# Performance work log

Measured on AMD Instinct MI355X. Metric: run time of the kernel, lower is better.

Reference implementation:

```python
import jax, jax.numpy as jnp
import numpy as np

H = 10            # forecast_horizon
DT = H / (H - 1)  # torchdiffeq 'rk4' steps on the linspace(0, H, H) grid
HID = 64


def setup_inputs() -> dict:
    key = jax.random.key(0)
    ks = jax.random.split(key, 7)
    x = jax.random.normal(ks[0], (1, 4096, 24), dtype=jnp.float32)
    # GCNConv params: out = A_hat @ (X W) + b
    W1 = jax.random.normal(ks[1], (1, HID), dtype=jnp.float32) * 0.5
    b1 = jax.random.normal(ks[2], (HID,), dtype=jnp.float32) * 0.1
    W2 = jax.random.normal(ks[3], (HID, HID), dtype=jnp.float32) * (1.0 / np.sqrt(HID))
    b2 = jax.random.normal(ks[4], (HID,), dtype=jnp.float32) * 0.1
    W3 = jax.random.normal(ks[5], (HID, 1), dtype=jnp.float32) * (1.0 / np.sqrt(HID))
    b3 = jax.random.normal(ks[6], (1,), dtype=jnp.float32) * 0.1
    return {"x": x, "W1": W1, "b1": b1, "W2": W2, "b2": b2, "W3": W3, "b3": b3}


def reference(x, W1, b1, W2, b2, W3, b3):
    B, N, T = x.shape  # B = 1, so the B*N state rows coincide with the N graph nodes
    M = B * N
    y0 = x[:, :, -1].reshape(M, 1)  # initial ODE state (B*N, F=1)

    def f(y):
        # GCNConv on a fully-connected graph with self-loops: every degree = M,
        # so A_hat = (1/M) * ones(M, M) and A_hat @ Z is the broadcasted mean of Z.
        h = jnp.mean(y @ W1, axis=0, keepdims=True) + b1  # (1, HID)
        h = jnp.tanh(h)
        h = jnp.mean(h @ W2, axis=0, keepdims=True) + b2  # rows identical -> mean is identity
        h = jnp.tanh(h)
        h = jnp.mean(h @ W3, axis=0, keepdims=True) + b3  # (1, 1)
        return jnp.broadcast_to(h, (M, h.shape[-1]))      # (M, 1)

    def step(y, _):
        # torchdiffeq fixed-step 'rk4' = 3/8-rule RK4 (rk4_alt_step_func); f is autonomous
        k1 = f(y)
        k2 = f(y + DT * k1 / 3.0)
        k3 = f(y + DT * (k2 - k1 / 3.0))
        k4 = f(y + DT * (k1 - k2 + k3))
        y = y + DT * (k1 + 3.0 * k2 + 3.0 * k3 + k4) / 8.0
        return y, y

    _, ys = jax.lax.scan(step, y0, None, length=H - 1)
    preds = jnp.concatenate([y0[None], ys], axis=0)  # (H, M, 1)
    # view(H, B, N, F).permute(1, 3, 2, 0).squeeze(1) with F=1 -> (B, N, H)
    out = preds.reshape(H, B, N).transpose(1, 2, 0)
    return out
```

## Files before the change

### kernel.cpp

```cpp
#include <hip/hip_runtime.h>

typedef _Float16 half2_t __attribute__((ext_vector_type(2)));
typedef _Float16 half8_t __attribute__((ext_vector_type(8)));

constexpr int M_NODES = 4096;
constexpr int T_IN    = 24;
constexpr int HIDN    = 64;
constexpr int HOR     = 10;

__device__ __forceinline__ float fast_tanh(float x) {
    float e = __builtin_amdgcn_exp2f(x * 2.8853900817779268f);
    return 1.f - 2.f * __builtin_amdgcn_rcpf(e + 1.f);
}

__device__ __forceinline__ float fdot2f16(half2_t a, half2_t b, float c) {
#if __has_builtin(__builtin_amdgcn_fdot2)
    return __builtin_amdgcn_fdot2(a, b, c, false);
#else
    return fmaf((float)a[0], (float)b[0], fmaf((float)a[1], (float)b[1], c));
#endif
}

template<int CTRL, int ROW_MASK>
__device__ __forceinline__ float dpp_add(float v) {
    int t = __builtin_amdgcn_update_dpp(0, __float_as_int(v), CTRL, ROW_MASK, 0xf, true);
    return v + __int_as_float(t);
}
__device__ __forceinline__ float wave_allsum(float v) {
    v = dpp_add<0x111, 0xf>(v);
    v = dpp_add<0x112, 0xf>(v);
    v = dpp_add<0x114, 0xf>(v);
    v = dpp_add<0x118, 0xf>(v);
    v = dpp_add<0x142, 0xa>(v);
    v = dpp_add<0x143, 0xc>(v);
    return __int_as_float(__builtin_amdgcn_readlane(__float_as_int(v), 63));
}

__global__ __launch_bounds__(256, 1) void fused_gode_kernel(
    const float* __restrict__ x,
    const float* __restrict__ W1, const float* __restrict__ b1,
    const float* __restrict__ W2, const float* __restrict__ b2,
    const float* __restrict__ W3, const float* __restrict__ b3,
    float* __restrict__ out)
{
    const int tid  = threadIdx.x;
    const int lane = tid & 63;
    const int wid  = tid >> 6;

    __shared__ float y0s[M_NODES];
    __shared__ float psum[256];
    __shared__ __align__(16) _Float16 h1h[HIDN];
    __shared__ float cs[HOR];

    float w2f[HIDN];
    float w1 = 0.f, bb1 = 0.f, bb2 = 0.f, w3 = 0.f, bb3 = 0.f;
    if (wid == 0) {
        #pragma unroll
        for (int i = 0; i < HIDN; ++i) w2f[i] = W2[i * HIDN + lane];
        w1  = W1[lane];
        bb1 = b1[lane];
        bb2 = b2[lane];
        w3  = W3[lane];
        bb3 = b3[0];
    }

    float msum = 0.f;
    #pragma unroll
    for (int k = 0; k < M_NODES / 256; ++k) {
        int n = tid + 256 * k;
        float v = x[n * T_IN + (T_IN - 1)];
        y0s[n] = v;
        msum += v;
    }
    psum[tid] = msum;
    __syncthreads();

    if (wid == 0) {
        float s = psum[lane] + psum[lane + 64] + psum[lane + 128] + psum[lane + 192];
        float mu = wave_allsum(s) * (1.0f / (float)M_NODES);

        half2_t w2h[HIDN / 2];
        #pragma unroll
        for (int i = 0; i < HIDN; i += 2)
            w2h[i / 2] = half2_t{(_Float16)w2f[i], (_Float16)w2f[i + 1]};

        auto feval = [&](float arg) -> float {
            float h1 = fast_tanh(arg);
            h1h[lane] = (_Float16)h1;
            __builtin_amdgcn_wave_barrier();
            const half8_t* hv = (const half8_t*)h1h;
            float acc[8];
            #pragma unroll
            for (int r = 0; r < 8; ++r) {
                half8_t u = hv[r];
                half2_t p0{u[0], u[1]}, p1{u[2], u[3]}, p2{u[4], u[5]}, p3{u[6], u[7]};
                float a = fdot2f16(p0, w2h[4 * r + 0], 0.f);
                a = fdot2f16(p1, w2h[4 * r + 1], a);
                a = fdot2f16(p2, w2h[4 * r + 2], a);
                acc[r] = fdot2f16(p3, w2h[4 * r + 3], a);
            }
            float h2 = fast_tanh((((acc[0] + acc[1]) + (acc[2] + acc[3])) +
                                  ((acc[4] + acc[5]) + (acc[6] + acc[7]))) + bb2);
            __builtin_amdgcn_wave_barrier();
            return wave_allsum(h2 * w3) + bb3;
        };

        const float DT  = (float)HOR / (float)(HOR - 1);
        const float dw  = DT * w1;
        const float dw3 = (DT * (1.f / 3.f)) * w1;

        float c = 0.f;
        if (lane == 0) cs[0] = 0.f;
        for (int t = 1; t < HOR; ++t) {
            float base = fmaf(mu, w1, bb1);
            float k1 = feval(base);
            float k2 = feval(fmaf(k1, dw3, base));
            float k3 = feval(fmaf(k2, dw, fmaf(k1, -dw3, base)));
            float k4 = feval(fmaf(k3, dw, fmaf(k1 - k2, dw, base)));
            float d  = DT * (k1 + 3.f * k2 + 3.f * k3 + k4) * 0.125f;
            mu += d;
            c  += d;
            if (lane == 0) cs[t] = c;
        }
    }
    __syncthreads();

    float4* out4 = (float4*)out;
    constexpr int NV4 = M_NODES * HOR / 4;
    #pragma unroll
    for (int k = 0; k < NV4 / 256; ++k) {
        int idx = tid + 256 * k;
        int e = idx * 4;
        int n = e / 10;
        int h = e - n * 10;
        float4 v;
        v.x = y0s[n] + cs[h]; if (++h == 10) { h = 0; ++n; }
        v.y = y0s[n] + cs[h]; if (++h == 10) { h = 0; ++n; }
        v.z = y0s[n] + cs[h]; if (++h == 10) { h = 0; ++n; }
        v.w = y0s[n] + cs[h];
        out4[idx] = v;
    }
}

extern "C" void kernel_launch(void* const* d_in, const int* in_sizes, int n_in,
                              void* d_out, int out_size, void* d_ws, size_t ws_size,
                              hipStream_t stream) {
    const float* x  = (const float*)d_in[0];
    const float* W1 = (const float*)d_in[1];
    const float* b1 = (const float*)d_in[2];
    const float* W2 = (const float*)d_in[3];
    const float* b2 = (const float*)d_in[4];
    const float* W3 = (const float*)d_in[5];
    const float* b3 = (const float*)d_in[6];
    float* out = (float*)d_out;

    fused_gode_kernel<<<1, 256, 0, stream>>>(x, W1, b1, W2, b2, W3, b3, out);
}
```

Baseline: 19.47 us.

## Split into partial-sum kernel and multi-block ODE solve with distributed output writes

```diff
diff --git a/kernel.cpp b/kernel.cpp
--- a/kernel.cpp
+++ b/kernel.cpp
@@ -7,6 +7,8 @@
 constexpr int T_IN    = 24;
 constexpr int HIDN    = 64;
 constexpr int HOR     = 10;
+constexpr int NB1     = 16;
+constexpr int NB2     = 64;
 
 __device__ __forceinline__ float fast_tanh(float x) {
     float e = __builtin_amdgcn_exp2f(x * 2.8853900817779268f);
@@ -36,8 +38,21 @@
     return __int_as_float(__builtin_amdgcn_readlane(__float_as_int(v), 63));
 }
 
-__global__ __launch_bounds__(256, 1) void fused_gode_kernel(
-    const float* __restrict__ x,
+__global__ __launch_bounds__(256) void partial_sum_kernel(
+    const float* __restrict__ x, float* __restrict__ partials)
+{
+    const int tid = threadIdx.x;
+    const int n   = blockIdx.x * 256 + tid;
+    float v = x[n * T_IN + (T_IN - 1)];
+    float s = wave_allsum(v);
+    __shared__ float ps[4];
+    if ((tid & 63) == 0) ps[tid >> 6] = s;
+    __syncthreads();
+    if (tid == 0) partials[blockIdx.x] = (ps[0] + ps[1]) + (ps[2] + ps[3]);
+}
+
+__global__ __launch_bounds__(256, 1) void ode_write_kernel(
+    const float* __restrict__ x, const float* __restrict__ partials,
     const float* __restrict__ W1, const float* __restrict__ b1,
     const float* __restrict__ W2, const float* __restrict__ b2,
     const float* __restrict__ W3, const float* __restrict__ b3,
@@ -47,37 +62,28 @@
     const int lane = tid & 63;
     const int wid  = tid >> 6;
 
-    __shared__ float y0s[M_NODES];
-    __shared__ float psum[256];
+    __shared__ float cs[HOR];
     __shared__ __align__(16) _Float16 h1h[HIDN];
-    __shared__ float cs[HOR];
+    __shared__ float ys[64 + 1];
 
-    float w2f[HIDN];
-    float w1 = 0.f, bb1 = 0.f, bb2 = 0.f, w3 = 0.f, bb3 = 0.f;
+    const int nbase = blockIdx.x * (M_NODES / NB2);
+    if (tid < 64) ys[tid] = x[(nbase + tid) * T_IN + (T_IN - 1)];
+
     if (wid == 0) {
+        float w2f[HIDN];
         #pragma unroll
         for (int i = 0; i < HIDN; ++i) w2f[i] = W2[i * HIDN + lane];
-        w1  = W1[lane];
-        bb1 = b1[lane];
-        bb2 = b2[lane];
-        w3  = W3[lane];
-        bb3 = b3[0];
-    }
+        const float w1  = W1[lane];
+        const float bb1 = b1[lane];
+        const float bb2 = b2[lane];
+        const float w3  = W3[lane];
+        const float bb3 = b3[0];
 
-    float msum = 0.f;
-    #pragma unroll
-    for (int k = 0; k < M_NODES / 256; ++k) {
-        int n = tid + 256 * k;
-        float v = x[n * T_IN + (T_IN - 1)];
-        y0s[n] = v;
-        msum += v;
-    }
-    psum[tid] = msum;
-    __syncthreads();
-
-    if (wid == 0) {
-        float s = psum[lane] + psum[lane + 64] + psum[lane + 128] + psum[lane + 192];
-        float mu = wave_allsum(s) * (1.0f / (float)M_NODES);
+        const float4* p4 = (const float4*)partials;
+        float4 pa = p4[0], pb = p4[1], pc = p4[2], pd = p4[3];
+        float mu = (((pa.x + pa.y) + (pa.z + pa.w)) + ((pb.x + pb.y) + (pb.z + pb.w)) +
+                    ((pc.x + pc.y) + (pc.z + pc.w)) + ((pd.x + pd.y) + (pd.z + pd.w)))
+                   * (1.0f / (float)M_NODES);
 
         half2_t w2h[HIDN / 2];
         #pragma unroll
@@ -125,20 +131,17 @@
     }
     __syncthreads();
 
-    float4* out4 = (float4*)out;
-    constexpr int NV4 = M_NODES * HOR / 4;
-    #pragma unroll
-    for (int k = 0; k < NV4 / 256; ++k) {
-        int idx = tid + 256 * k;
-        int e = idx * 4;
+    constexpr int NF4 = (M_NODES / NB2) * HOR / 4;
+    if (tid < NF4) {
+        int e = tid * 4;
         int n = e / 10;
         int h = e - n * 10;
         float4 v;
-        v.x = y0s[n] + cs[h]; if (++h == 10) { h = 0; ++n; }
-        v.y = y0s[n] + cs[h]; if (++h == 10) { h = 0; ++n; }
-        v.z = y0s[n] + cs[h]; if (++h == 10) { h = 0; ++n; }
-        v.w = y0s[n] + cs[h];
-        out4[idx] = v;
+        v.x = ys[n] + cs[h]; if (++h == 10) { h = 0; ++n; }
+        v.y = ys[n] + cs[h]; if (++h == 10) { h = 0; ++n; }
+        v.z = ys[n] + cs[h]; if (++h == 10) { h = 0; ++n; }
+        v.w = ys[n] + cs[h];
+        ((float4*)(out + nbase * HOR))[tid] = v;
     }
 }
 
@@ -152,7 +155,9 @@
     const float* b2 = (const float*)d_in[4];
     const float* W3 = (const float*)d_in[5];
     const float* b3 = (const float*)d_in[6];
-    float* out = (float*)d_out;
+    float* out      = (float*)d_out;
+    float* partials = (float*)d_ws;
 
-    fused_gode_kernel<<<1, 256, 0, stream>>>(x, W1, b1, W2, b2, W3, b3, out);
+    partial_sum_kernel<<<NB1, 256, 0, stream>>>(x, partials);
+    ode_write_kernel<<<NB2, 256, 0, stream>>>(x, partials, W1, b1, W2, b2, W3, b3, out);
 }
```

New measurement: 19.88 us. +2.1%, slower.

## Replicate ODE solve across 64 blocks, each writing its own node slice

Applied to the files above, without the earlier changes.

```diff
diff --git a/kernel.cpp b/kernel.cpp
--- a/kernel.cpp
+++ b/kernel.cpp
@@ -7,6 +7,7 @@
 constexpr int T_IN    = 24;
 constexpr int HIDN    = 64;
 constexpr int HOR     = 10;
+constexpr int NB      = 64;
 
 __device__ __forceinline__ float fast_tanh(float x) {
     float e = __builtin_amdgcn_exp2f(x * 2.8853900817779268f);
@@ -47,10 +48,12 @@
     const int lane = tid & 63;
     const int wid  = tid >> 6;
 
-    __shared__ float y0s[M_NODES];
     __shared__ float psum[256];
+    __shared__ float cs[HOR];
     __shared__ __align__(16) _Float16 h1h[HIDN];
-    __shared__ float cs[HOR];
+    __shared__ float ys[64 + 1];
+
+    const int nbase = blockIdx.x * (M_NODES / NB);
 
     float w2f[HIDN];
     float w1 = 0.f, bb1 = 0.f, bb2 = 0.f, w3 = 0.f, bb3 = 0.f;
@@ -63,21 +66,18 @@
         w3  = W3[lane];
         bb3 = b3[0];
     }
+    if (wid == 1) ys[lane] = x[(nbase + lane) * T_IN + (T_IN - 1)];
 
-    float msum = 0.f;
+    float s = 0.f;
     #pragma unroll
-    for (int k = 0; k < M_NODES / 256; ++k) {
-        int n = tid + 256 * k;
-        float v = x[n * T_IN + (T_IN - 1)];
-        y0s[n] = v;
-        msum += v;
-    }
-    psum[tid] = msum;
+    for (int k = 0; k < M_NODES / 256; ++k)
+        s += x[(tid + 256 * k) * T_IN + (T_IN - 1)];
+    psum[tid] = s;
     __syncthreads();
 
     if (wid == 0) {
-        float s = psum[lane] + psum[lane + 64] + psum[lane + 128] + psum[lane + 192];
-        float mu = wave_allsum(s) * (1.0f / (float)M_NODES);
+        float t4 = psum[lane] + psum[lane + 64] + psum[lane + 128] + psum[lane + 192];
+        float mu = wave_allsum(t4) * (1.0f / (float)M_NODES);
 
         half2_t w2h[HIDN / 2];
         #pragma unroll
@@ -125,20 +125,17 @@
     }
     __syncthreads();
 
-    float4* out4 = (float4*)out;
-    constexpr int NV4 = M_NODES * HOR / 4;
-    #pragma unroll
-    for (int k = 0; k < NV4 / 256; ++k) {
-        int idx = tid + 256 * k;
-        int e = idx * 4;
+    constexpr int NF4 = (M_NODES / NB) * HOR / 4;
+    if (tid < NF4) {
+        int e = tid * 4;
         int n = e / 10;
         int h = e - n * 10;
         float4 v;
-        v.x = y0s[n] + cs[h]; if (++h == 10) { h = 0; ++n; }
-        v.y = y0s[n] + cs[h]; if (++h == 10) { h = 0; ++n; }
-        v.z = y0s[n] + cs[h]; if (++h == 10) { h = 0; ++n; }
-        v.w = y0s[n] + cs[h];
-        out4[idx] = v;
+        v.x = ys[n] + cs[h]; if (++h == 10) { h = 0; ++n; }
+        v.y = ys[n] + cs[h]; if (++h == 10) { h = 0; ++n; }
+        v.z = ys[n] + cs[h]; if (++h == 10) { h = 0; ++n; }
+        v.w = ys[n] + cs[h];
+        ((float4*)(out + nbase * HOR))[tid] = v;
     }
 }
 
@@ -154,5 +151,5 @@
     const float* b3 = (const float*)d_in[6];
     float* out = (float*)d_out;
 
-    fused_gode_kernel<<<1, 256, 0, stream>>>(x, W1, b1, W2, b2, W3, b3, out);
+    fused_gode_kernel<<<NB, 256, 0, stream>>>(x, W1, b1, W2, b2, W3, b3, out);
 }
```

New measurement: 17.25 us. 1.13x faster.
